# Kernel optimization log

Measured on AMD Instinct MI355X. Metric: run time of the kernel, lower is better.

Reference implementation:

```python
import jax, jax.numpy as jnp
import numpy as np

# dims
B, T, N, E, ENC, HID, HEADS, D = 64, 128, 2000, 300, 256, 256, 5, 16
IN = ENC + 2 * E          # GRUCell input: assign_emb + program_emb + node_emb
ATT = HID * HEADS         # self-attention context dim (Lin et al. 2017 multi-head)


def setup_inputs() -> dict:
    key = jax.random.key(0)
    ks = jax.random.split(key, 16)
    f = lambda k, shp, s=0.05: jax.random.normal(k, shp, dtype=jnp.float32) * s
    return {
        "program_emb": f(ks[0], (B, ENC), 1.0),
        "h0": f(ks[1], (B, HID), 1.0),                 # xavier-like init h0
        "node_emb": f(ks[2], (N + 1, E)),              # nn.Embedding(num_nodes+1, E)
        "label_emb": f(ks[3], (N + 1, D, E)),          # per-node label embedding experts
        "gru_w_ih": f(ks[4], (3 * HID, IN)),
        "gru_w_hh": f(ks[5], (3 * HID, HID)),
        "gru_b_ih": f(ks[6], (3 * HID,)),
        "gru_b_hh": f(ks[7], (3 * HID,)),
        "attn_ws1": f(ks[8], (HID, HID)),              # SelfAttention ws1 (no bias)
        "attn_ws2": f(ks[9], (HEADS, HID)),            # SelfAttention ws2 (no bias)
        "pred_w": f(ks[10], (N + 1, ATT, D)),          # per-node Linear experts
        "pred_b": f(ks[11], (N + 1, D)),
        "execution_trace": jax.random.randint(ks[12], (B, T), 0, N + 1),
        "node_assignments": jax.random.randint(ks[13], (B, N), 0, D),
        "execution_lengths": jax.random.randint(ks[14], (B,), 1, T + 1),
    }


def _forward(program_emb, h0, node_emb, label_emb, gru_w_ih, gru_w_hh,
             gru_b_ih, gru_b_hh, attn_ws1, attn_ws2, pred_w, pred_b,
             execution_trace, node_assignments):
    # pad assignments with a zero column (PAD node indexes column N)
    na = jnp.concatenate(
        [node_assignments, jnp.zeros((B, 1), node_assignments.dtype)], axis=1)
    rows = jnp.arange(B)
    pos = jnp.arange(T - 1)

    def step(carry, xs):
        h, store = carry
        node_i, node_ip1, i = xs
        # routed label-embedding lookup: expert chosen by node id, row by assignment
        assign_emb = label_emb[node_i, na[rows, node_i]]        # [B,E]
        x = jnp.concatenate([assign_emb, program_emb, node_emb[node_i]], axis=1)
        # torch nn.GRUCell math
        gi = x @ gru_w_ih.T + gru_b_ih
        gh = h @ gru_w_hh.T + gru_b_hh
        ir, iz, inn = jnp.split(gi, 3, axis=1)
        hr, hz, hn = jnp.split(gh, 3, axis=1)
        r = jax.nn.sigmoid(ir + hr)
        z = jax.nn.sigmoid(iz + hz)
        n = jnp.tanh(inn + r * hn)
        h = (1.0 - z) * n + z * h
        # append to growing hidden_store (fixed buffer, step-i slot)
        store = jax.lax.dynamic_update_slice_in_dim(store, h[:, None, :], i, axis=1)
        # structured self-attention over all stored hiddens.
        # NOTE: attn_lengths = max(exec_len, len(store)) >= len(store), so the
        # length mask never hides any stored position; only unwritten slots mask.
        scores = jnp.tanh(store @ attn_ws1.T) @ attn_ws2.T      # [B,T-1,HEADS]
        scores = jnp.where((pos <= i)[None, :, None], scores, -1e9)
        alpha = jax.nn.softmax(scores, axis=1)                  # softmax over time
        ctx = jnp.einsum('bth,btd->bhd', alpha, store).reshape(B, ATT)
        # routed prediction head: expert chosen by next node id (grouped GEMM)
        out = jnp.einsum('bd,bdk->bk', ctx, pred_w[node_ip1]) + pred_b[node_ip1]
        return (h, store), (out, alpha)

    store0 = jnp.zeros((B, T - 1, HID), h0.dtype)
    xs = (execution_trace[:, :-1].T, execution_trace[:, 1:].T, jnp.arange(T - 1))
    (_, _), (outs, alphas) = jax.lax.scan(step, (h0, store0), xs)
    return outs, alphas  # [T-1,B,D], [T-1,B,T-1,HEADS]


def reference(program_emb, h0, node_emb, label_emb, gru_w_ih, gru_w_hh,
              gru_b_ih, gru_b_hh, attn_ws1, attn_ws2, pred_w, pred_b,
              execution_trace, node_assignments, execution_lengths):
    # execution_lengths only enters via max(exec_len, step+1) which never masks;
    # kept for interface fidelity.
    del execution_lengths
    return _forward(program_emb, h0, node_emb, label_emb, gru_w_ih, gru_w_hh,
                    gru_b_ih, gru_b_hh, attn_ws1, attn_ws2, pred_w, pred_b,
                    execution_trace, node_assignments)
```

## Files before the change

### kernel.cpp

```cpp
#include <hip/hip_runtime.h>
#include <hip/hip_bf16.h>
#include <math.h>

#define BB 64
#define TT 128
#define T1 127
#define NNODE 2000
#define EE 300
#define HID 256
#define NHEADS 5
#define DD 16
#define G3 768
#define ATT 1280
#define SCALE_H 28.0f

typedef _Float16 h2_t __attribute__((ext_vector_type(2)));
typedef short short8 __attribute__((ext_vector_type(8)));
typedef float f32x4 __attribute__((ext_vector_type(4)));

__device__ __forceinline__ int dot4(int a, int b, int c) {
#if __has_builtin(__builtin_amdgcn_sdot4)
    return __builtin_amdgcn_sdot4(a, b, c, false);
#else
    int r;
    asm("v_dot4_i32_i8 %0, %1, %2, %3" : "=v"(r) : "v"(a), "v"(b), "v"(c));
    return r;
#endif
}

__device__ __forceinline__ unsigned short f2bf(float f) {
    unsigned u = __float_as_uint(f);
    unsigned r = (u + 0x7FFFu + ((u >> 16) & 1u)) >> 16;
    return (unsigned short)r;
}

__global__ void k_tcvt(const float* __restrict__ src, unsigned short* __restrict__ dst, int R, int C) {
    int idx = blockIdx.x * 256 + threadIdx.x;
    if (idx < R * C) {
        int r = idx / C, c = idx % C;
        dst[c * R + r] = f2bf(src[idx]);
    }
}

__global__ __launch_bounds__(64) void k_quant(const float* __restrict__ w, int* __restrict__ wq,
                                              float* __restrict__ wsc) {
    int row = blockIdx.x;
    int t = threadIdx.x;
    const float* wr = w + (size_t)row * HID;
    float4 v = *(const float4*)(wr + t * 4);
    float m = fmaxf(fmaxf(fabsf(v.x), fabsf(v.y)), fmaxf(fabsf(v.z), fabsf(v.w)));
#pragma unroll
    for (int off = 1; off < 64; off <<= 1) m = fmaxf(m, __shfl_xor(m, off));
    float s = (m > 0.f) ? m * (1.0f / 127.0f) : 1.0f;
    float inv = 1.0f / s;
    int q0 = max(-127, min(127, __float2int_rn(v.x * inv)));
    int q1 = max(-127, min(127, __float2int_rn(v.y * inv)));
    int q2 = max(-127, min(127, __float2int_rn(v.z * inv)));
    int q3 = max(-127, min(127, __float2int_rn(v.w * inv)));
    wq[row * 64 + t] = (q0 & 0xFF) | ((q1 & 0xFF) << 8) | ((q2 & 0xFF) << 16) | ((q3 & 0xFF) << 24);
    if (t == 0) wsc[row] = s;
}

__global__ __launch_bounds__(256) void k_mgemm(
    const float* __restrict__ A, const unsigned short* __restrict__ B16,
    float* __restrict__ out, const float* __restrict__ bias,
    const int* __restrict__ trace, const int* __restrict__ na,
    int mode, int M, int K, int N, int strideA, int ntiles, int brow0, int Bld, int dotanh)
{
    __shared__ short As[64][40];
    __shared__ short Bt[64][40];
    __shared__ int baseLds[64];
    __shared__ int validLds[64];
    int tid = threadIdx.x;
    int bm = blockIdx.x / ntiles, bn = blockIdx.x % ntiles;
    int m0 = bm * 64, n0 = bn * 64;
    if (tid < 64) {
        int m = m0 + tid;
        int valid = (m < M) ? 1 : 0;
        int base = 0;
        if (valid) {
            if (mode == 2) {
                int i = m >> 6, bb = m & 63;
                int node = trace[bb * TT + i];
                int asg = (node < NNODE) ? na[bb * NNODE + node] : 0;
                base = (node * DD + asg) * EE;
            } else {
                base = m * strideA;
            }
        }
        baseLds[tid] = base;
        validLds[tid] = valid;
    }
    __syncthreads();

    int wv = tid >> 6, l = tid & 63;
    int lr = l & 15, lg = l >> 4;
    f32x4 acc[4];
#pragma unroll
    for (int cb = 0; cb < 4; cb++) acc[cb] = (f32x4){0.f, 0.f, 0.f, 0.f};

    int ar = tid >> 2, aq = tid & 3;
    int bk = tid >> 3, bq = tid & 7;
    int nsteps = (K + 31) >> 5;
    for (int it = 0; it < nsteps; it++) {
        int kk = it * 32;
        {
            int base = baseLds[ar], val = validLds[ar];
            short8 t1;
#pragma unroll
            for (int j = 0; j < 8; j++) {
                int kx = kk + aq * 8 + j;
                float v = (val && kx < K) ? A[(size_t)base + kx] : 0.f;
                t1[j] = (short)f2bf(v);
            }
            *(short8*)&As[ar][aq * 8] = t1;
        }
        {
            int kx = kk + bk;
            short8 t2;
            if (kx < K) {
                t2 = *(const short8*)(B16 + (size_t)(brow0 + kx) * Bld + n0 + bq * 8);
            } else {
#pragma unroll
                for (int j = 0; j < 8; j++) t2[j] = 0;
            }
#pragma unroll
            for (int j = 0; j < 8; j++) Bt[bq * 8 + j][bk] = t2[j];
        }
        __syncthreads();
        short8 a = *(const short8*)&As[wv * 16 + lr][lg * 8];
#pragma unroll
        for (int cb = 0; cb < 4; cb++) {
            short8 bfr = *(const short8*)&Bt[cb * 16 + lr][lg * 8];
            acc[cb] = __builtin_amdgcn_mfma_f32_16x16x32_bf16(a, bfr, acc[cb], 0, 0, 0);
        }
        __syncthreads();
    }
#pragma unroll
    for (int cb = 0; cb < 4; cb++) {
        int col = n0 + cb * 16 + lr;
#pragma unroll
        for (int q = 0; q < 4; q++) {
            int row = m0 + wv * 16 + lg * 4 + q;
            if (row < M) {
                float v = acc[cb][q];
                if (bias) v += bias[col];
                if (dotanh) v = tanhf(v);
                out[(size_t)row * N + col] = v;
            }
        }
    }
}

#define LG_PITCH 328
__global__ __launch_bounds__(256) void k_lgemm2(
    const float* __restrict__ A, const unsigned short* __restrict__ B16,
    const float* __restrict__ node_t, const float* __restrict__ prog_t,
    const int* __restrict__ trace, const int* __restrict__ na,
    float* __restrict__ out)
{
    __shared__ short Afull[64][LG_PITCH];
    __shared__ short Bt[64][40];
    __shared__ int nodeLds[64];
    const int tid = threadIdx.x;
    const int ib = blockIdx.x >> 2;
    const int npg = blockIdx.x & 3;

    if (tid < 64) nodeLds[tid] = trace[tid * TT + ib];
    __syncthreads();

#pragma unroll
    for (int g = 0; g < 10; g++) {
        int idx = tid + g * 256;
        int row = idx / 40, c8 = idx % 40;
        int node = nodeLds[row];
        int asg = (node < NNODE) ? na[row * NNODE + node] : 0;
        const float* ap = A + (size_t)(node * DD + asg) * EE;
        short8 t1;
#pragma unroll
        for (int j = 0; j < 8; j++) {
            int kx = c8 * 8 + j;
            float v = (kx < EE) ? ap[kx] : 0.f;
            t1[j] = (short)f2bf(v);
        }
        *(short8*)&Afull[row][c8 * 8] = t1;
    }
    __syncthreads();

    const int wv = tid >> 6, l = tid & 63;
    const int lr = l & 15, lg = l >> 4;
    const int bk = tid >> 3, bq = tid & 7;

    for (int np = npg * 3; np < npg * 3 + 3; np++) {
        int n0 = np * 64;
        f32x4 acc[4];
#pragma unroll
        for (int cb = 0; cb < 4; cb++) acc[cb] = (f32x4){0.f, 0.f, 0.f, 0.f};
#pragma unroll
        for (int ks = 0; ks < 10; ks++) {
            int kx = ks * 32 + bk;
            short8 t2;
            if (kx < EE) {
                t2 = *(const short8*)(B16 + (size_t)kx * G3 + n0 + bq * 8);
            } else {
#pragma unroll
                for (int j = 0; j < 8; j++) t2[j] = 0;
            }
#pragma unroll
            for (int j = 0; j < 8; j++) Bt[bq * 8 + j][bk] = t2[j];
            __syncthreads();
            short8 a = *(const short8*)&Afull[wv * 16 + lr][ks * 32 + lg * 8];
#pragma unroll
            for (int cb = 0; cb < 4; cb++) {
                short8 bfr = *(const short8*)&Bt[cb * 16 + lr][lg * 8];
                acc[cb] = __builtin_amdgcn_mfma_f32_16x16x32_bf16(a, bfr, acc[cb], 0, 0, 0);
            }
            __syncthreads();
        }
#pragma unroll
        for (int cb = 0; cb < 4; cb++) {
            int col = n0 + cb * 16 + lr;
#pragma unroll
            for (int q = 0; q < 4; q++) {
                int rl = wv * 16 + lg * 4 + q;
                int node = nodeLds[rl];
                float v = acc[cb][q] + node_t[(size_t)node * G3 + col] + prog_t[(size_t)rl * G3 + col];
                out[((size_t)ib * 64 + rl) * G3 + col] = v;
            }
        }
    }
}

__global__ __launch_bounds__(512, 2) void rec9_kernel(
    const float* __restrict__ h0, const int* __restrict__ whh8q, const float* __restrict__ wsc,
    const float* __restrict__ bhh, const float* __restrict__ gsum, float* __restrict__ store)
{
    __shared__ float hs32[HID];
    __shared__ int hs8w[HID / 4];
    const int tid = threadIdx.x;
    const int s = tid & 1;
    const int k = tid >> 1;
    const int b = blockIdx.x;

    if (tid < HID) {
        float v = h0[(size_t)b * HID + tid];
        hs32[tid] = v;
        int q = max(-127, min(127, __float2int_rn(v * SCALE_H)));
        ((char*)hs8w)[tid] = (char)q;
    }

    int wR[32], wZ[32], wN[32];
    {
        const int* pr = whh8q + (size_t)k * 64 + s * 32;
        const int* pz = whh8q + (size_t)(HID + k) * 64 + s * 32;
        const int* pn = whh8q + (size_t)(2 * HID + k) * 64 + s * 32;
#pragma unroll
        for (int cc = 0; cc < 32; cc++) { wR[cc] = pr[cc]; wZ[cc] = pz[cc]; wN[cc] = pn[cc]; }
    }
    const float sR = wsc[k] * (1.0f / SCALE_H);
    const float sZ = wsc[HID + k] * (1.0f / SCALE_H);
    const float sN = wsc[2 * HID + k] * (1.0f / SCALE_H);
    const float bhr = bhh[k], bhz = bhh[HID + k], bhn = bhh[2 * HID + k];
    __syncthreads();

    float gr_c = 0.f, gz_c = 0.f, gn_c = 0.f;
    if (s == 0) {
        const float* lp = gsum + (size_t)b * G3;
        gr_c = lp[k]; gz_c = lp[HID + k]; gn_c = lp[2 * HID + k];
    }

    for (int i = 0; i < T1; i++) {
        float gr_n = 0.f, gz_n = 0.f, gn_n = 0.f;
        if (s == 0 && i + 1 < T1) {
            const float* lp = gsum + ((size_t)(i + 1) * BB + b) * G3;
            gr_n = lp[k]; gz_n = lp[HID + k]; gn_n = lp[2 * HID + k];
        }
        int ar = 0, az = 0, an = 0;
#pragma unroll
        for (int cc = 0; cc < 32; cc++) {
            int hv = hs8w[s * 32 + cc];
            ar = dot4(wR[cc], hv, ar);
            az = dot4(wZ[cc], hv, az);
            an = dot4(wN[cc], hv, an);
        }
        ar += __shfl_xor(ar, 1); az += __shfl_xor(az, 1); an += __shfl_xor(an, 1);
        __syncthreads();
        if (s == 0) {
            float arf = (float)ar * sR, azf = (float)az * sZ, anf = (float)an * sN;
            float r = 1.f / (1.f + expf(-(gr_c + arf + bhr)));
            float z = 1.f / (1.f + expf(-(gz_c + azf + bhz)));
            float n = tanhf(gn_c + r * (anf + bhn));
            float hold = hs32[k];
            float hnew = (1.f - z) * n + z * hold;
            hs32[k] = hnew;
            store[((size_t)b * T1 + i) * HID + k] = hnew;
            int q = max(-127, min(127, __float2int_rn(hnew * SCALE_H)));
            ((char*)hs8w)[k] = (char)q;
        }
        __syncthreads();
        gr_c = gr_n; gz_c = gz_n; gn_c = gn_n;
    }
}

__global__ void k_scores(const float* __restrict__ U, const float* __restrict__ ws2, float* __restrict__ sbuf) {
    int flat = blockIdx.x * 256 + threadIdx.x;
    if (flat < BB * T1 * NHEADS) {
        int m = flat / NHEADS, h = flat % NHEADS;
        const float* u = U + (size_t)m * HID;
        const float* w = ws2 + h * HID;
        float acc = 0.f;
        for (int c = 0; c < HID; c += 4) {
            float4 u4 = *(const float4*)(u + c);
            float4 w4 = *(const float4*)(w + c);
            acc += u4.x * w4.x + u4.y * w4.y + u4.z * w4.z + u4.w * w4.w;
        }
        sbuf[flat] = acc;
    }
}

__global__ __launch_bounds__(128) void k_softmax_par(const float* __restrict__ sbuf,
                                                     float* __restrict__ ebuf, float* __restrict__ rD) {
    __shared__ float a[128];
    int bh = blockIdx.x;
    int b = bh / NHEADS, h = bh % NHEADS;
    int t = threadIdx.x;
    const float* sp = sbuf + (size_t)b * T1 * NHEADS + h;
    float sv = (t < T1) ? sp[t * NHEADS] : -1e30f;
    a[t] = sv;
    __syncthreads();
#pragma unroll
    for (int off = 64; off >= 1; off >>= 1) {
        if (t < off) a[t] = fmaxf(a[t], a[t + off]);
        __syncthreads();
    }
    float m = a[0];
    __syncthreads();
    float e = (t < T1) ? expf(sv - m) : 0.f;
    a[t] = e;
#pragma unroll
    for (int off = 1; off < 128; off <<= 1) {
        __syncthreads();
        float v = (t >= off) ? a[t - off] : 0.f;
        __syncthreads();
        a[t] += v;
    }
    if (t < T1) {
        ebuf[(b * T1 + t) * NHEADS + h] = e;
        rD[(b * T1 + t) * NHEADS + h] = 1.f / a[t];
    }
}

__global__ void k_alphas(const float* __restrict__ ebuf, const float* __restrict__ rD, float* __restrict__ alph) {
    int flat = blockIdx.x * 256 + threadIdx.x;
    const int TOT = T1 * BB * T1 * NHEADS;
    if (flat < TOT) {
        int i = flat / (BB * T1 * NHEADS);
        int rem = flat % (BB * T1 * NHEADS);
        int b = rem / (T1 * NHEADS);
        int rem2 = rem % (T1 * NHEADS);
        int t = rem2 / NHEADS, h = rem2 % NHEADS;
        float v = 0.f;
        if (t <= i) v = ebuf[(b * T1 + t) * NHEADS + h] * rD[(b * T1 + i) * NHEADS + h];
        alph[flat] = v;
    }
}

__global__ __launch_bounds__(256) void k_ctx(const float* __restrict__ ebuf, const float* __restrict__ rD,
                                             const float* __restrict__ store, float* __restrict__ ctx) {
    __shared__ float eL[T1], rL[T1];
    int b = blockIdx.x / NHEADS, h = blockIdx.x % NHEADS;
    int k = threadIdx.x;
    if (k < T1) {
        eL[k] = ebuf[(b * T1 + k) * NHEADS + h];
        rL[k] = rD[(b * T1 + k) * NHEADS + h];
    }
    __syncthreads();
    float acc = 0.f;
#pragma unroll 4
    for (int t = 0; t < T1; t++) {
        acc += eL[t] * store[((size_t)b * T1 + t) * HID + k];
        ctx[((size_t)t * BB + b) * ATT + h * HID + k] = acc * rL[t];
    }
}

__global__ void k_count(const int* __restrict__ trace, int* __restrict__ cnt) {
    int idx = blockIdx.x * 256 + threadIdx.x;
    if (idx < T1 * BB) {
        int i = idx >> 6, b = idx & 63;
        int node = trace[b * TT + i + 1];
        atomicAdd(&cnt[node], 1);
    }
}

__global__ __launch_bounds__(256) void k_scan(const int* __restrict__ cnt, int* __restrict__ boff) {
    __shared__ int part[256];
    int t = threadIdx.x;
    int s0 = 0;
#pragma unroll
    for (int j = 0; j < 8; j++) { int idx = t * 8 + j; if (idx < NNODE + 1) s0 += cnt[idx]; }
    part[t] = s0;
    __syncthreads();
    for (int off = 1; off < 256; off <<= 1) {
        int u = (t >= off) ? part[t - off] : 0;
        __syncthreads();
        part[t] += u;
        __syncthreads();
    }
    int run = part[t] - s0;
    for (int j = 0; j < 8; j++) {
        int idx = t * 8 + j;
        if (idx < NNODE + 1) { boff[idx] = run; run += cnt[idx]; }
    }
    if (t == 255) boff[NNODE + 1] = part[255];
}

__global__ void k_scatter(const int* __restrict__ trace, const int* __restrict__ boff,
                          int* __restrict__ cur, int* __restrict__ items) {
    int idx = blockIdx.x * 256 + threadIdx.x;
    if (idx < T1 * BB) {
        int i = idx >> 6, b = idx & 63;
        int node = trace[b * TT + i + 1];
        int pos = atomicAdd(&cur[node], 1);
        items[boff[node] + pos] = idx;
    }
}

__global__ __launch_bounds__(256) void k_pred2(
    const float* __restrict__ ctx, const float* __restrict__ pw, const float* __restrict__ pb,
    const int* __restrict__ boff, const int* __restrict__ items, float* __restrict__ outs)
{
    __shared__ float cl[8][ATT];
    __shared__ float red[16][16][8];
    int e = blockIdx.x;
    int start = boff[e], end = boff[e + 1];
    if (start == end) return;
    int tid = threadIdx.x;
    int d = tid & 15, ks = tid >> 4;
    const float* w = pw + (size_t)e * ATT * DD;
    float biasv = pb[e * DD + d];
    for (int c0 = start; c0 < end; c0 += 8) {
        int cn = min(8, end - c0);
        for (int j = 0; j < cn; j++) {
            int item = items[c0 + j];
            const float* cp = ctx + (size_t)item * ATT;
            for (int x = tid; x < ATT; x += 256) cl[j][x] = cp[x];
        }
        __syncthreads();
        float acc[8];
#pragma unroll
        for (int j = 0; j < 8; j++) acc[j] = 0.f;
        for (int kx = ks * 80; kx < ks * 80 + 80; kx++) {
            float wv = w[kx * DD + d];
#pragma unroll
            for (int j = 0; j < 8; j++) acc[j] += cl[j][kx] * wv;
        }
#pragma unroll
        for (int j = 0; j < 8; j++) red[ks][d][j] = acc[j];
        __syncthreads();
#pragma unroll
        for (int st = 8; st >= 1; st >>= 1) {
            if (ks < st) {
#pragma unroll
                for (int j = 0; j < 8; j++) red[ks][d][j] += red[ks + st][d][j];
            }
            __syncthreads();
        }
        if (ks == 0) {
            for (int j = 0; j < cn; j++) {
                int item = items[c0 + j];
                outs[(size_t)item * DD + d] = red[0][d][j] + biasv;
            }
        }
        __syncthreads();
    }
}

extern "C" void kernel_launch(void* const* d_in, const int* in_sizes, int n_in,
                              void* d_out, int out_size, void* d_ws, size_t ws_size,
                              hipStream_t stream) {
    const float* program_emb = (const float*)d_in[0];
    const float* h0       = (const float*)d_in[1];
    const float* node_emb = (const float*)d_in[2];
    const float* label_emb= (const float*)d_in[3];
    const float* w_ih     = (const float*)d_in[4];
    const float* w_hh     = (const float*)d_in[5];
    const float* b_ih     = (const float*)d_in[6];
    const float* b_hh     = (const float*)d_in[7];
    const float* ws1      = (const float*)d_in[8];
    const float* ws2      = (const float*)d_in[9];
    const float* pred_w   = (const float*)d_in[10];
    const float* pred_b   = (const float*)d_in[11];
    const int*   trace    = (const int*)d_in[12];
    const int*   na       = (const int*)d_in[13];

    float*          ws      = (float*)d_ws;
    float*          store   = ws + 0;
    unsigned short* wihT16  = (unsigned short*)(ws + 2080768);
    unsigned short* ws1T16  = (unsigned short*)(ws + 2409472);
    float*          prog_t  = ws + 2803712;
    float*          node_t  = ws + 2852864;
    float*          sbuf    = ws + 4389632;
    float*          ebuf    = ws + 4430272;
    float*          rD      = ws + 4470912;
    float*          label_p = ws + 4511568;
    float*          Ubuf    = ws + 10753872;
    int*            whh8q   = (int*)(ws + 12834640);
    float*          wsc     = ws + 12883792;
    float*          ctx     = ws + 4511568;
    int*            cnt     = (int*)(ws + 2080768);
    int*            cur     = cnt + 2048;
    int*            boff    = cur + 2048;
    int*            items   = boff + 2048;

    float* outs = (float*)d_out;
    float* alph = outs + T1 * BB * DD;

    k_tcvt<<<2568, 256, 0, stream>>>(w_ih, wihT16, G3, 856);
    k_tcvt<<<256, 256, 0, stream>>>(ws1, ws1T16, HID, HID);
    k_quant<<<G3, 64, 0, stream>>>(w_hh, whh8q, wsc);
    k_mgemm<<<12,   256, 0, stream>>>(program_emb, wihT16, prog_t, b_ih,   nullptr, nullptr, 0, 64,   256, G3,  256, 12, 300, G3, 0);
    k_mgemm<<<384,  256, 0, stream>>>(node_emb,    wihT16, node_t, nullptr, nullptr, nullptr, 0, 2001, 300, G3,  300, 12, 556, G3, 0);
    k_lgemm2<<<508, 256, 0, stream>>>(label_emb, wihT16, node_t, prog_t, trace, na, label_p);

    rec9_kernel<<<64, 512, 0, stream>>>(h0, whh8q, wsc, b_hh, label_p, store);

    k_mgemm<<<508, 256, 0, stream>>>(store, ws1T16, Ubuf, nullptr, nullptr, nullptr, 0, 8128, 256, HID, 256, 4, 0, HID, 1);
    k_scores<<<159, 256, 0, stream>>>(Ubuf, ws2, sbuf);
    k_softmax_par<<<BB * NHEADS, 128, 0, stream>>>(sbuf, ebuf, rD);
    k_alphas<<<20162, 256, 0, stream>>>(ebuf, rD, alph);
    k_ctx<<<320, 256, 0, stream>>>(ebuf, rD, store, ctx);

    hipMemsetAsync(cnt, 0, 2 * 2048 * sizeof(int), stream);
    k_count<<<32, 256, 0, stream>>>(trace, cnt);
    k_scan<<<1, 256, 0, stream>>>(cnt, boff);
    k_scatter<<<32, 256, 0, stream>>>(trace, boff, cur, items);
    k_pred2<<<NNODE + 1, 256, 0, stream>>>(ctx, pred_w, pred_b, boff, items, outs);
}
```

Measured before the change: 372.0 us.

## Merge setup and bucketing kernels, vectorize recurrence weights, store ctx as bf16

```diff
diff --git a/kernel.cpp b/kernel.cpp
--- a/kernel.cpp
+++ b/kernel.cpp
@@ -34,11 +34,19 @@
     return (unsigned short)r;
 }
 
-__global__ void k_tcvt(const float* __restrict__ src, unsigned short* __restrict__ dst, int R, int C) {
+__global__ void k_tcvt2(const float* __restrict__ a, unsigned short* __restrict__ da, int Ra, int Ca,
+                        const float* __restrict__ b, unsigned short* __restrict__ db, int Rb, int Cb) {
     int idx = blockIdx.x * 256 + threadIdx.x;
-    if (idx < R * C) {
-        int r = idx / C, c = idx % C;
-        dst[c * R + r] = f2bf(src[idx]);
+    int na = Ra * Ca;
+    if (idx < na) {
+        int r = idx / Ca, c = idx % Ca;
+        da[c * Ra + r] = f2bf(a[idx]);
+    } else {
+        idx -= na;
+        if (idx < Rb * Cb) {
+            int r = idx / Cb, c = idx % Cb;
+            db[c * Rb + r] = f2bf(b[idx]);
+        }
     }
 }
 
@@ -231,7 +239,7 @@
     }
 }
 
-__global__ __launch_bounds__(512, 2) void rec9_kernel(
+__global__ __launch_bounds__(512, 2) void rec10_kernel(
     const float* __restrict__ h0, const int* __restrict__ whh8q, const float* __restrict__ wsc,
     const float* __restrict__ bhh, const float* __restrict__ gsum, float* __restrict__ store)
 {
@@ -249,13 +257,13 @@
         ((char*)hs8w)[tid] = (char)q;
     }
 
-    int wR[32], wZ[32], wN[32];
+    int4 wR[8], wZ[8], wN[8];
     {
-        const int* pr = whh8q + (size_t)k * 64 + s * 32;
-        const int* pz = whh8q + (size_t)(HID + k) * 64 + s * 32;
-        const int* pn = whh8q + (size_t)(2 * HID + k) * 64 + s * 32;
-#pragma unroll
-        for (int cc = 0; cc < 32; cc++) { wR[cc] = pr[cc]; wZ[cc] = pz[cc]; wN[cc] = pn[cc]; }
+        const int4* pr = (const int4*)(whh8q + (size_t)k * 64 + s * 32);
+        const int4* pz = (const int4*)(whh8q + (size_t)(HID + k) * 64 + s * 32);
+        const int4* pn = (const int4*)(whh8q + (size_t)(2 * HID + k) * 64 + s * 32);
+#pragma unroll
+        for (int c8 = 0; c8 < 8; c8++) { wR[c8] = pr[c8]; wZ[c8] = pz[c8]; wN[c8] = pn[c8]; }
     }
     const float sR = wsc[k] * (1.0f / SCALE_H);
     const float sZ = wsc[HID + k] * (1.0f / SCALE_H);
@@ -277,11 +285,16 @@
         }
         int ar = 0, az = 0, an = 0;
 #pragma unroll
-        for (int cc = 0; cc < 32; cc++) {
-            int hv = hs8w[s * 32 + cc];
-            ar = dot4(wR[cc], hv, ar);
-            az = dot4(wZ[cc], hv, az);
-            an = dot4(wN[cc], hv, an);
+        for (int c8 = 0; c8 < 8; c8++) {
+            int4 wr = wR[c8], wz = wZ[c8], wn = wN[c8];
+            int hv0 = hs8w[s * 32 + c8 * 4 + 0];
+            int hv1 = hs8w[s * 32 + c8 * 4 + 1];
+            int hv2 = hs8w[s * 32 + c8 * 4 + 2];
+            int hv3 = hs8w[s * 32 + c8 * 4 + 3];
+            ar = dot4(wr.x, hv0, ar); az = dot4(wz.x, hv0, az); an = dot4(wn.x, hv0, an);
+            ar = dot4(wr.y, hv1, ar); az = dot4(wz.y, hv1, az); an = dot4(wn.y, hv1, an);
+            ar = dot4(wr.z, hv2, ar); az = dot4(wz.z, hv2, az); an = dot4(wn.z, hv2, an);
+            ar = dot4(wr.w, hv3, ar); az = dot4(wz.w, hv3, az); an = dot4(wn.w, hv3, an);
         }
         ar += __shfl_xor(ar, 1); az += __shfl_xor(az, 1); an += __shfl_xor(an, 1);
         __syncthreads();
@@ -366,7 +379,7 @@
 }
 
 __global__ __launch_bounds__(256) void k_ctx(const float* __restrict__ ebuf, const float* __restrict__ rD,
-                                             const float* __restrict__ store, float* __restrict__ ctx) {
+                                             const float* __restrict__ store, unsigned short* __restrict__ ctx16) {
     __shared__ float eL[T1], rL[T1];
     int b = blockIdx.x / NHEADS, h = blockIdx.x % NHEADS;
     int k = threadIdx.x;
@@ -379,54 +392,57 @@
 #pragma unroll 4
     for (int t = 0; t < T1; t++) {
         acc += eL[t] * store[((size_t)b * T1 + t) * HID + k];
-        ctx[((size_t)t * BB + b) * ATT + h * HID + k] = acc * rL[t];
-    }
-}
-
-__global__ void k_count(const int* __restrict__ trace, int* __restrict__ cnt) {
-    int idx = blockIdx.x * 256 + threadIdx.x;
-    if (idx < T1 * BB) {
+        ctx16[((size_t)t * BB + b) * ATT + h * HID + k] = f2bf(acc * rL[t]);
+    }
+}
+
+__global__ __launch_bounds__(1024) void k_bucket(const int* __restrict__ trace,
+                                                 int* __restrict__ boff, int* __restrict__ items) {
+    __shared__ int cnt[NNODE + 1];
+    __shared__ int cur[NNODE + 1];
+    __shared__ int part[256];
+    int t = threadIdx.x;
+    for (int x = t; x < NNODE + 1; x += 1024) cnt[x] = 0;
+    __syncthreads();
+    for (int idx = t; idx < T1 * BB; idx += 1024) {
         int i = idx >> 6, b = idx & 63;
         int node = trace[b * TT + i + 1];
         atomicAdd(&cnt[node], 1);
     }
-}
-
-__global__ __launch_bounds__(256) void k_scan(const int* __restrict__ cnt, int* __restrict__ boff) {
-    __shared__ int part[256];
-    int t = threadIdx.x;
+    __syncthreads();
     int s0 = 0;
-#pragma unroll
-    for (int j = 0; j < 8; j++) { int idx = t * 8 + j; if (idx < NNODE + 1) s0 += cnt[idx]; }
-    part[t] = s0;
+    if (t < 256) {
+#pragma unroll
+        for (int j = 0; j < 8; j++) { int idx = t * 8 + j; if (idx < NNODE + 1) s0 += cnt[idx]; }
+        part[t] = s0;
+    }
     __syncthreads();
     for (int off = 1; off < 256; off <<= 1) {
-        int u = (t >= off) ? part[t - off] : 0;
-        __syncthreads();
-        part[t] += u;
-        __syncthreads();
-    }
-    int run = part[t] - s0;
-    for (int j = 0; j < 8; j++) {
-        int idx = t * 8 + j;
-        if (idx < NNODE + 1) { boff[idx] = run; run += cnt[idx]; }
-    }
-    if (t == 255) boff[NNODE + 1] = part[255];
-}
-
-__global__ void k_scatter(const int* __restrict__ trace, const int* __restrict__ boff,
-                          int* __restrict__ cur, int* __restrict__ items) {
-    int idx = blockIdx.x * 256 + threadIdx.x;
-    if (idx < T1 * BB) {
+        int u = 0;
+        if (t < 256 && t >= off) u = part[t - off];
+        __syncthreads();
+        if (t < 256) part[t] += u;
+        __syncthreads();
+    }
+    if (t < 256) {
+        int run = part[t] - s0;
+        for (int j = 0; j < 8; j++) {
+            int idx = t * 8 + j;
+            if (idx < NNODE + 1) { boff[idx] = run; cur[idx] = run; run += cnt[idx]; }
+        }
+        if (t == 255) boff[NNODE + 1] = part[255];
+    }
+    __syncthreads();
+    for (int idx = t; idx < T1 * BB; idx += 1024) {
         int i = idx >> 6, b = idx & 63;
         int node = trace[b * TT + i + 1];
         int pos = atomicAdd(&cur[node], 1);
-        items[boff[node] + pos] = idx;
+        items[pos] = idx;
     }
 }
 
 __global__ __launch_bounds__(256) void k_pred2(
-    const float* __restrict__ ctx, const float* __restrict__ pw, const float* __restrict__ pb,
+    const unsigned short* __restrict__ ctx16, const float* __restrict__ pw, const float* __restrict__ pb,
     const int* __restrict__ boff, const int* __restrict__ items, float* __restrict__ outs)
 {
     __shared__ float cl[8][ATT];
@@ -442,8 +458,9 @@
         int cn = min(8, end - c0);
         for (int j = 0; j < cn; j++) {
             int item = items[c0 + j];
-            const float* cp = ctx + (size_t)item * ATT;
-            for (int x = tid; x < ATT; x += 256) cl[j][x] = cp[x];
+            const unsigned short* cp = ctx16 + (size_t)item * ATT;
+            for (int x = tid; x < ATT; x += 256)
+                cl[j][x] = __uint_as_float((unsigned)cp[x] << 16);
         }
         __syncthreads();
         float acc[8];
@@ -506,33 +523,28 @@
     float*          Ubuf    = ws + 10753872;
     int*            whh8q   = (int*)(ws + 12834640);
     float*          wsc     = ws + 12883792;
-    float*          ctx     = ws + 4511568;
-    int*            cnt     = (int*)(ws + 2080768);
-    int*            cur     = cnt + 2048;
-    int*            boff    = cur + 2048;
+    unsigned short* ctx16   = (unsigned short*)(ws + 4511568);
+    int*            cnt_    = (int*)(ws + 2080768);
+    int*            boff    = cnt_ + 4096;
     int*            items   = boff + 2048;
 
     float* outs = (float*)d_out;
     float* alph = outs + T1 * BB * DD;
 
-    k_tcvt<<<2568, 256, 0, stream>>>(w_ih, wihT16, G3, 856);
-    k_tcvt<<<256, 256, 0, stream>>>(ws1, ws1T16, HID, HID);
+    k_tcvt2<<<2824, 256, 0, stream>>>(w_ih, wihT16, G3, 856, ws1, ws1T16, HID, HID);
     k_quant<<<G3, 64, 0, stream>>>(w_hh, whh8q, wsc);
     k_mgemm<<<12,   256, 0, stream>>>(program_emb, wihT16, prog_t, b_ih,   nullptr, nullptr, 0, 64,   256, G3,  256, 12, 300, G3, 0);
     k_mgemm<<<384,  256, 0, stream>>>(node_emb,    wihT16, node_t, nullptr, nullptr, nullptr, 0, 2001, 300, G3,  300, 12, 556, G3, 0);
     k_lgemm2<<<508, 256, 0, stream>>>(label_emb, wihT16, node_t, prog_t, trace, na, label_p);
 
-    rec9_kernel<<<64, 512, 0, stream>>>(h0, whh8q, wsc, b_hh, label_p, store);
+    rec10_kernel<<<64, 512, 0, stream>>>(h0, whh8q, wsc, b_hh, label_p, store);
 
     k_mgemm<<<508, 256, 0, stream>>>(store, ws1T16, Ubuf, nullptr, nullptr, nullptr, 0, 8128, 256, HID, 256, 4, 0, HID, 1);
     k_scores<<<159, 256, 0, stream>>>(Ubuf, ws2, sbuf);
     k_softmax_par<<<BB * NHEADS, 128, 0, stream>>>(sbuf, ebuf, rD);
     k_alphas<<<20162, 256, 0, stream>>>(ebuf, rD, alph);
-    k_ctx<<<320, 256, 0, stream>>>(ebuf, rD, store, ctx);
-
-    hipMemsetAsync(cnt, 0, 2 * 2048 * sizeof(int), stream);
-    k_count<<<32, 256, 0, stream>>>(trace, cnt);
-    k_scan<<<1, 256, 0, stream>>>(cnt, boff);
-    k_scatter<<<32, 256, 0, stream>>>(trace, boff, cur, items);
-    k_pred2<<<NNODE + 1, 256, 0, stream>>>(ctx, pred_w, pred_b, boff, items, outs);
-}
+    k_ctx<<<320, 256, 0, stream>>>(ebuf, rD, store, ctx16);
+
+    k_bucket<<<1, 1024, 0, stream>>>(trace, boff, items);
+    k_pred2<<<NNODE + 1, 256, 0, stream>>>(ctx16, pred_w, pred_b, boff, items, outs);
+}
```

Result: no change. 372.6 us (+0.1%).
